# Kernel tuning notes

Measured on AMD Instinct MI355X. Metric: run time of the kernel, lower is better.

## Reference

```python
import jax, jax.numpy as jnp
import numpy as np

B, T, D = 4, 2048, 1024

def setup_inputs() -> dict:
    key = jax.random.key(0)
    kx, kq, kk, kv = jax.random.split(key, 4)
    return {
        "vector": jax.random.normal(kx, (B, T, D), dtype=jnp.float32),
        # original uses torch.rand -> uniform [0,1)
        "W_queries": jax.random.uniform(kq, (D, D), dtype=jnp.float32),
        "W_keys": jax.random.uniform(kk, (D, D), dtype=jnp.float32),
        "W_values": jax.random.uniform(kv, (D, D), dtype=jnp.float32),
    }

def reference(vector, W_queries, W_keys, W_values):
    b, num_token, d_out = vector.shape
    queries = vector @ W_queries          # [b, t, d]
    keys = vector @ W_keys                # [b, t, d]
    values = vector @ W_values            # [b, t, d]
    # attention_score: [b, q, k]
    scores = jnp.einsum('bqd,bkd->bqk', queries, keys)
    causal_mask = jnp.triu(jnp.ones((num_token, num_token), dtype=bool), k=1)
    scores = jnp.where(causal_mask[None, :, :], -jnp.inf, scores)
    # NOTE: original uses FLOOR division `//` by sqrt(d_k) -- faithful here.
    inv_sqrt_scale = jnp.asarray(np.sqrt(keys.shape[-1]), dtype=scores.dtype)
    weights = jnp.floor(scores / inv_sqrt_scale)
    # NOTE: original applies softmax over dim=1 (the query axis), not dim=-1.
    weights = jax.nn.softmax(weights, axis=1)
    # dropout rate is 0.0 (eval/deterministic): identity
    context = jnp.einsum('bqk,bkd->bqd', weights, values)
    return context
```

## Files before the change

kernel.cpp:

```cpp
#include <hip/hip_runtime.h>
#include <math.h>

typedef _Float16 half4 __attribute__((ext_vector_type(4)));
typedef _Float16 half8 __attribute__((ext_vector_type(8)));
typedef float f32x4 __attribute__((ext_vector_type(4)));

#define GLD16(gptr, lptr)                                                     \
    __builtin_amdgcn_global_load_lds(                                         \
        (const __attribute__((address_space(1))) unsigned int*)(gptr),        \
        (__attribute__((address_space(3))) unsigned int*)(lptr), 16, 0, 0)

namespace {

constexpr int Bb = 4;
constexpr int Tt = 2048;
constexpr int Dd = 1024;
constexpr int BT = Bb * Tt;
constexpr int NCH = 16;

__device__ inline _Float16 f2h(float f) { return (_Float16)f; }

__global__ __launch_bounds__(256) void convert_x_kernel(
    const float* __restrict__ X, _Float16* __restrict__ Xhi, _Float16* __restrict__ Xlo)
{
    const int idx = (blockIdx.x * 256 + threadIdx.x) * 4;
    const float4 v = *(const float4*)(X + idx);
    const float a[4] = {v.x, v.y, v.z, v.w};
    half4 h, l;
#pragma unroll
    for (int i = 0; i < 4; ++i) {
        h[i] = f2h(a[i]);
        l[i] = f2h(a[i] - (float)h[i]);
    }
    *(half4*)(Xhi + idx) = h;
    *(half4*)(Xlo + idx) = l;
}

__global__ __launch_bounds__(256) void convert_wqk_kernel(
    const float* __restrict__ Wq, const float* __restrict__ Wk,
    _Float16* __restrict__ Wqh, _Float16* __restrict__ Wql,
    _Float16* __restrict__ Wkh, _Float16* __restrict__ Wkl)
{
    const int mat = blockIdx.y;
    const float* W = mat ? Wk : Wq;
    _Float16* Hh = mat ? Wkh : Wqh;
    _Float16* Ll = mat ? Wkl : Wql;
    const int idx = (blockIdx.x * 256 + threadIdx.x) * 4;
    const float4 v = *(const float4*)(W + idx);
    const float a[4] = {v.x, v.y, v.z, v.w};
    half4 h, l;
#pragma unroll
    for (int i = 0; i < 4; ++i) {
        h[i] = f2h(a[i]);
        l[i] = f2h(a[i] - (float)h[i]);
    }
    *(half4*)(Hh + idx) = h;
    *(half4*)(Ll + idx) = l;
}

__global__ __launch_bounds__(256) void convert_wv_kernel(
    const float* __restrict__ Wv, _Float16* __restrict__ WvTh)
{
    __shared__ float tile[64][65];
    const int n0 = blockIdx.x * 64, k0 = blockIdx.y * 64;
    const int tx = threadIdx.x & 63, ty = threadIdx.x >> 6;
#pragma unroll
    for (int i = 0; i < 16; ++i)
        tile[ty + i * 4][tx] = Wv[(size_t)(k0 + ty + i * 4) * Dd + n0 + tx];
    __syncthreads();
#pragma unroll
    for (int i = 0; i < 16; ++i) {
        const float v = tile[tx][ty + i * 4];
        WvTh[(size_t)(n0 + ty + i * 4) * Dd + k0 + tx] = f2h(v);
    }
}

__global__ __launch_bounds__(256) void gt_kernel(
    const _Float16* __restrict__ Wkh, const _Float16* __restrict__ Wkl,
    const _Float16* __restrict__ Wqh, const _Float16* __restrict__ Wql,
    _Float16* __restrict__ GTh, _Float16* __restrict__ GTl)
{
    __shared__ _Float16 Ahl[2][4][512];
    __shared__ _Float16 Bhl[2][4][512];

    const int n0 = blockIdx.x * 64;
    const int m0 = blockIdx.y * 64;
    const int tid = threadIdx.x;
    const int w = tid >> 6, lane = tid & 63;
    const int lr = lane & 15, lq = lane >> 4;
    const int wi = (w >> 1) * 2, wj = (w & 1) * 2;

    f32x4 acc[2][2];
#pragma unroll
    for (int i = 0; i < 2; ++i)
#pragma unroll
        for (int j = 0; j < 2; ++j)
#pragma unroll
            for (int c = 0; c < 4; ++c) acc[i][j][c] = 0.f;

    for (int kk = 0; kk < 1024; kk += 32) {
        __syncthreads();
        {
            const int s = w;
            const size_t ar = (size_t)(m0 + s * 16 + lr) * Dd + kk + lq * 8;
            const size_t br = (size_t)(n0 + s * 16 + lr) * Dd + kk + lq * 8;
            GLD16(Wkh + ar, &Ahl[0][s][0]);
            GLD16(Wkl + ar, &Ahl[1][s][0]);
            GLD16(Wqh + br, &Bhl[0][s][0]);
            GLD16(Wql + br, &Bhl[1][s][0]);
        }
        __syncthreads();
        half8 ah[2], al[2], bh[2], bl[2];
#pragma unroll
        for (int i = 0; i < 2; ++i) {
            ah[i] = *(const half8*)&Ahl[0][wi + i][lane * 8];
            al[i] = *(const half8*)&Ahl[1][wi + i][lane * 8];
        }
#pragma unroll
        for (int j = 0; j < 2; ++j) {
            bh[j] = *(const half8*)&Bhl[0][wj + j][lane * 8];
            bl[j] = *(const half8*)&Bhl[1][wj + j][lane * 8];
        }
#pragma unroll
        for (int i = 0; i < 2; ++i)
#pragma unroll
            for (int j = 0; j < 2; ++j) {
                acc[i][j] = __builtin_amdgcn_mfma_f32_16x16x32_f16(ah[i], bh[j], acc[i][j], 0, 0, 0);
                acc[i][j] = __builtin_amdgcn_mfma_f32_16x16x32_f16(ah[i], bl[j], acc[i][j], 0, 0, 0);
                acc[i][j] = __builtin_amdgcn_mfma_f32_16x16x32_f16(al[i], bh[j], acc[i][j], 0, 0, 0);
            }
    }

#pragma unroll
    for (int i = 0; i < 2; ++i)
#pragma unroll
        for (int r = 0; r < 4; ++r) {
            const int row = m0 + (wi + i) * 16 + lq * 4 + r;
#pragma unroll
            for (int j = 0; j < 2; ++j) {
                const int col = n0 + (wj + j) * 16 + lr;
                const float v = acc[i][j][r];
                const _Float16 h = f2h(v);
                GTh[(size_t)row * Dd + col] = h;
                GTl[(size_t)row * Dd + col] = f2h(v - (float)h);
            }
        }
}

__global__ __launch_bounds__(256) void t_kernel(
    const _Float16* __restrict__ Xhi, const _Float16* __restrict__ Xlo,
    const _Float16* __restrict__ GTh, const _Float16* __restrict__ GTl,
    _Float16* __restrict__ Thi, _Float16* __restrict__ Tlo)
{
    __shared__ _Float16 Ahl[2][8][512];
    __shared__ _Float16 Bhl[2][8][512];

    const int n0 = blockIdx.x * 128;
    const int m0 = blockIdx.y * 128;
    const int tid = threadIdx.x;
    const int w = tid >> 6, lane = tid & 63;
    const int lr = lane & 15, lq = lane >> 4;
    const int wr = (w >> 1) * 4, wc = (w & 1) * 4;

    f32x4 acc[4][4];
#pragma unroll
    for (int i = 0; i < 4; ++i)
#pragma unroll
        for (int j = 0; j < 4; ++j)
#pragma unroll
            for (int c = 0; c < 4; ++c) acc[i][j][c] = 0.f;

    for (int kk = 0; kk < 1024; kk += 32) {
        __syncthreads();
#pragma unroll
        for (int s2 = 0; s2 < 2; ++s2) {
            const int s = w * 2 + s2;
            const size_t ar = (size_t)(m0 + s * 16 + lr) * Dd + kk + lq * 8;
            const size_t br = (size_t)(n0 + s * 16 + lr) * Dd + kk + lq * 8;
            GLD16(Xhi + ar, &Ahl[0][s][0]);
            GLD16(Xlo + ar, &Ahl[1][s][0]);
            GLD16(GTh + br, &Bhl[0][s][0]);
            GLD16(GTl + br, &Bhl[1][s][0]);
        }
        __syncthreads();
        half8 ah[4], al[4], bh[4], bl[4];
#pragma unroll
        for (int i = 0; i < 4; ++i) {
            ah[i] = *(const half8*)&Ahl[0][wr + i][lane * 8];
            al[i] = *(const half8*)&Ahl[1][wr + i][lane * 8];
        }
#pragma unroll
        for (int j = 0; j < 4; ++j) {
            bh[j] = *(const half8*)&Bhl[0][wc + j][lane * 8];
            bl[j] = *(const half8*)&Bhl[1][wc + j][lane * 8];
        }
#pragma unroll
        for (int i = 0; i < 4; ++i)
#pragma unroll
            for (int j = 0; j < 4; ++j) {
                acc[i][j] = __builtin_amdgcn_mfma_f32_16x16x32_f16(ah[i], bh[j], acc[i][j], 0, 0, 0);
                acc[i][j] = __builtin_amdgcn_mfma_f32_16x16x32_f16(ah[i], bl[j], acc[i][j], 0, 0, 0);
                acc[i][j] = __builtin_amdgcn_mfma_f32_16x16x32_f16(al[i], bh[j], acc[i][j], 0, 0, 0);
            }
    }
#pragma unroll
    for (int i = 0; i < 4; ++i)
#pragma unroll
        for (int r = 0; r < 4; ++r) {
            const int row = m0 + (wr + i) * 16 + lq * 4 + r;
#pragma unroll
            for (int j = 0; j < 4; ++j) {
                const int col = n0 + (wc + j) * 16 + lr;
                const float v = acc[i][j][r];
                const _Float16 h = f2h(v);
                Thi[(size_t)row * Dd + col] = h;
                Tlo[(size_t)row * Dd + col] = f2h(v - (float)h);
            }
        }
}

__global__ __launch_bounds__(256) void v_kernel(
    const _Float16* __restrict__ Xhi, const _Float16* __restrict__ WvTh,
    _Float16* __restrict__ Vrow)
{
    __shared__ _Float16 Al[8][512];
    __shared__ _Float16 Bl[8][512];

    const int n0 = blockIdx.x * 128;
    const int m0 = blockIdx.y * 128;
    const int tid = threadIdx.x;
    const int w = tid >> 6, lane = tid & 63;
    const int lr = lane & 15, lq = lane >> 4;
    const int wr = (w >> 1) * 4, wc = (w & 1) * 4;

    f32x4 acc[4][4];
#pragma unroll
    for (int i = 0; i < 4; ++i)
#pragma unroll
        for (int j = 0; j < 4; ++j)
#pragma unroll
            for (int c = 0; c < 4; ++c) acc[i][j][c] = 0.f;

    for (int kk = 0; kk < 1024; kk += 32) {
        __syncthreads();
#pragma unroll
        for (int s2 = 0; s2 < 2; ++s2) {
            const int s = w * 2 + s2;
            GLD16(Xhi + (size_t)(m0 + s * 16 + lr) * Dd + kk + lq * 8, &Al[s][0]);
            GLD16(WvTh + (size_t)(n0 + s * 16 + lr) * Dd + kk + lq * 8, &Bl[s][0]);
        }
        __syncthreads();
        half8 a[4], b2[4];
#pragma unroll
        for (int i = 0; i < 4; ++i) a[i] = *(const half8*)&Al[wr + i][lane * 8];
#pragma unroll
        for (int j = 0; j < 4; ++j) b2[j] = *(const half8*)&Bl[wc + j][lane * 8];
#pragma unroll
        for (int i = 0; i < 4; ++i)
#pragma unroll
            for (int j = 0; j < 4; ++j)
                acc[i][j] = __builtin_amdgcn_mfma_f32_16x16x32_f16(a[i], b2[j], acc[i][j], 0, 0, 0);
    }
#pragma unroll
    for (int i = 0; i < 4; ++i)
#pragma unroll
        for (int r = 0; r < 4; ++r) {
            const int row = m0 + (wr + i) * 16 + lq * 4 + r;
#pragma unroll
            for (int j = 0; j < 4; ++j)
                Vrow[(size_t)row * Dd + n0 + (wc + j) * 16 + lr] = f2h(acc[i][j][r]);
        }
}

__global__ __launch_bounds__(256) void transpose_v_kernel(
    const _Float16* __restrict__ Vrow, const float* __restrict__ Lb,
    _Float16* __restrict__ Vt)
{
    __shared__ _Float16 tile[64][78];
    const int d0 = blockIdx.x * 64, t0 = blockIdx.y * 64, b = blockIdx.z;
    const int tx = threadIdx.x & 63, ty = threadIdx.x >> 6;
#pragma unroll
    for (int i = 0; i < 16; ++i)
        tile[ty + i * 4][tx] = Vrow[((size_t)b * Tt + t0 + ty + i * 4) * Dd + d0 + tx];
    __syncthreads();
    const float sc = Lb[(size_t)b * Tt + t0 + tx];
#pragma unroll
    for (int i = 0; i < 16; ++i) {
        const float v = (float)tile[tx][ty + i * 4] * sc;
        Vt[(size_t)b * Dd * Tt + (size_t)(d0 + ty + i * 4) * Tt + t0 + tx] = f2h(v);
    }
}

__global__ __launch_bounds__(256) void scores_mfma_kernel(
    const _Float16* __restrict__ Thi, const _Float16* __restrict__ Tlo,
    const _Float16* __restrict__ Xhi, const _Float16* __restrict__ Xlo,
    float* __restrict__ S, float* __restrict__ Pm, float* __restrict__ Pl)
{
    const int t = blockIdx.x;
    int byi = (int)((sqrtf(8.f * t + 1.f) - 1.f) * 0.5f);
    if ((byi + 1) * (byi + 2) / 2 <= t) ++byi;
    if (byi * (byi + 1) / 2 > t) --byi;
    const int bxi = t - byi * (byi + 1) / 2;
    const int b = blockIdx.z;
    const int j0 = bxi * 128, q0 = byi * 128;
    float* Sb = S + (size_t)b * Tt * Tt;

    __shared__ _Float16 Ahl[2][8][512];
    __shared__ _Float16 Bhl[2][8][512];
    const _Float16* Th = Thi + (size_t)b * Tt * Dd;
    const _Float16* Tl = Tlo + (size_t)b * Tt * Dd;
    const _Float16* Xh = Xhi + (size_t)b * Tt * Dd;
    const _Float16* Xl = Xlo + (size_t)b * Tt * Dd;

    const int tid = threadIdx.x;
    const int w = tid >> 6, lane = tid & 63;
    const int lr = lane & 15, lq = lane >> 4;
    const int wr = (w >> 1) * 4, wc = (w & 1) * 4;

    f32x4 acc[4][4];
#pragma unroll
    for (int i = 0; i < 4; ++i)
#pragma unroll
        for (int j = 0; j < 4; ++j)
#pragma unroll
            for (int c = 0; c < 4; ++c) acc[i][j][c] = 0.f;

    for (int kk = 0; kk < 1024; kk += 32) {
        __syncthreads();
#pragma unroll
        for (int s2 = 0; s2 < 2; ++s2) {
            const int s = w * 2 + s2;
            const size_t ar = (size_t)(q0 + s * 16 + lr) * Dd + kk + lq * 8;
            const size_t br = (size_t)(j0 + s * 16 + lr) * Dd + kk + lq * 8;
            GLD16(Th + ar, &Ahl[0][s][0]);
            GLD16(Tl + ar, &Ahl[1][s][0]);
            GLD16(Xh + br, &Bhl[0][s][0]);
            GLD16(Xl + br, &Bhl[1][s][0]);
        }
        __syncthreads();
        half8 ah[4], al[4], bh[4], bl[4];
#pragma unroll
        for (int i = 0; i < 4; ++i) {
            ah[i] = *(const half8*)&Ahl[0][wr + i][lane * 8];
            al[i] = *(const half8*)&Ahl[1][wr + i][lane * 8];
        }
#pragma unroll
        for (int j = 0; j < 4; ++j) {
            bh[j] = *(const half8*)&Bhl[0][wc + j][lane * 8];
            bl[j] = *(const half8*)&Bhl[1][wc + j][lane * 8];
        }
#pragma unroll
        for (int i = 0; i < 4; ++i)
#pragma unroll
            for (int j = 0; j < 4; ++j) {
                acc[i][j] = __builtin_amdgcn_mfma_f32_16x16x32_f16(ah[i], bh[j], acc[i][j], 0, 0, 0);
                acc[i][j] = __builtin_amdgcn_mfma_f32_16x16x32_f16(ah[i], bl[j], acc[i][j], 0, 0, 0);
                acc[i][j] = __builtin_amdgcn_mfma_f32_16x16x32_f16(al[i], bh[j], acc[i][j], 0, 0, 0);
            }
    }

    float sv[4][4][4];
#pragma unroll
    for (int i = 0; i < 4; ++i)
#pragma unroll
        for (int r = 0; r < 4; ++r) {
            const int q = q0 + (wr + i) * 16 + lq * 4 + r;
#pragma unroll
            for (int j = 0; j < 4; ++j) {
                const int jg = j0 + (wc + j) * 16 + lr;
                const float v = (jg <= q) ? floorf(acc[i][j][r] * 0.03125f) : -INFINITY;
                sv[i][j][r] = v;
                Sb[(size_t)q * Tt + jg] = v;
            }
        }

    float* red  = (float*)&Ahl[0][0][0];
    float* colm = red + 2048;
    __syncthreads();
    for (int e = tid; e < 2048; e += 256) red[e] = -INFINITY;
    __syncthreads();
    const int rowidx = (w * 4 + lq) * 128;
#pragma unroll
    for (int j = 0; j < 4; ++j) {
        const int c = (wc + j) * 16 + lr;
        float lm = -INFINITY;
#pragma unroll
        for (int i = 0; i < 4; ++i)
#pragma unroll
            for (int r = 0; r < 4; ++r) lm = fmaxf(lm, sv[i][j][r]);
        red[rowidx + c] = lm;
    }
    __syncthreads();
    if (tid < 128) {
        float m = -INFINITY;
#pragma unroll
        for (int e = 0; e < 16; ++e) m = fmaxf(m, red[e * 128 + tid]);
        colm[tid] = m;
    }
    __syncthreads();
    float ls[4];
#pragma unroll
    for (int j = 0; j < 4; ++j) {
        const int c = (wc + j) * 16 + lr;
        const float m = colm[c];
        float s = 0.f;
#pragma unroll
        for (int i = 0; i < 4; ++i)
#pragma unroll
            for (int r = 0; r < 4; ++r)
                if (sv[i][j][r] != -INFINITY) s += __expf(sv[i][j][r] - m);
        ls[j] = s;
    }
    __syncthreads();
    for (int e = tid; e < 2048; e += 256) red[e] = 0.f;
    __syncthreads();
#pragma unroll
    for (int j = 0; j < 4; ++j) red[rowidx + (wc + j) * 16 + lr] = ls[j];
    __syncthreads();
    if (tid < 128) {
        float l = 0.f;
#pragma unroll
        for (int e = 0; e < 16; ++e) l += red[e * 128 + tid];
        const size_t o = ((size_t)b * NCH + byi) * Tt + j0 + tid;
        Pm[o] = colm[tid];
        Pl[o] = l;
    }
}

__global__ __launch_bounds__(256) void colstats_merge_kernel(
    const float* __restrict__ Pm, const float* __restrict__ Pl,
    float* __restrict__ Mb, float* __restrict__ Lb)
{
    const int j = blockIdx.x * 256 + threadIdx.x;
    const int b = blockIdx.y;
    const int jt = j >> 7;
    float m = -INFINITY, l = 0.f;
    for (int c = jt; c < NCH; ++c) {
        const size_t pidx = ((size_t)b * NCH + c) * Tt + j;
        const float mi = Pm[pidx];
        if (mi == -INFINITY) continue;
        const float li = Pl[pidx];
        if (mi > m) { l = l * __expf(m - mi) + li; m = mi; }
        else        { l += li * __expf(mi - m); }
    }
    Mb[(size_t)b * Tt + j] = m;
    Lb[(size_t)b * Tt + j] = (l > 0.f) ? 1.f / l : 0.f;
}

__global__ __launch_bounds__(256) void pmat_kernel(
    const float* __restrict__ S, const float* __restrict__ Mb,
    _Float16* __restrict__ P)
{
    const int t = blockIdx.x;
    int byi = (int)((sqrtf(8.f * t + 1.f) - 1.f) * 0.5f);
    if ((byi + 1) * (byi + 2) / 2 <= t) ++byi;
    if (byi * (byi + 1) / 2 > t) --byi;
    const int bxi = t - byi * (byi + 1) / 2;
    const int b = blockIdx.z;
    const int j0 = bxi * 128, q0 = byi * 128;

    const int tr = threadIdx.x >> 4;
    const int tc = (threadIdx.x & 15) * 8;
    const float* mp = Mb + (size_t)b * Tt + j0 + tc;
    float mv[8];
#pragma unroll
    for (int e = 0; e < 8; ++e) mv[e] = mp[e];

#pragma unroll
    for (int it = 0; it < 8; ++it) {
        const int row = q0 + it * 16 + tr;
        const float* Sp = S + (size_t)b * Tt * Tt + (size_t)row * Tt + j0 + tc;
        const float4 s0 = *(const float4*)Sp;
        const float4 s1 = *(const float4*)(Sp + 4);
        const float sa[8] = {s0.x, s0.y, s0.z, s0.w, s1.x, s1.y, s1.z, s1.w};
        half8 out;
#pragma unroll
        for (int e = 0; e < 8; ++e) {
            const int jg = j0 + tc + e;
            out[e] = (jg <= row) ? f2h(__expf(sa[e] - mv[e])) : (_Float16)0.f;
        }
        *(half8*)(P + (size_t)b * Tt * Tt + (size_t)row * Tt + j0 + tc) = out;
    }
}

__global__ __launch_bounds__(256) void context_mfma_kernel(
    const _Float16* __restrict__ P, const _Float16* __restrict__ Vt,
    float* __restrict__ Out)
{
    __shared__ _Float16 Al[8][512];
    __shared__ _Float16 Bl[8][512];

    const int bx = blockIdx.x;
    const int by = (int)gridDim.y - 1 - blockIdx.y;
    const int b  = blockIdx.z;
    const int d0 = bx * 128;
    const int q0 = by * 128;
    const _Float16* Pb = P + (size_t)b * Tt * Tt;
    const _Float16* Vb = Vt + (size_t)b * Dd * Tt;
    float* Ob = Out + (size_t)b * Tt * Dd;

    const int tid = threadIdx.x;
    const int w = tid >> 6, lane = tid & 63;
    const int lr = lane & 15, lq = lane >> 4;
    const int wr = (w >> 1) * 4, wc = (w & 1) * 4;

    f32x4 acc[4][4];
#pragma unroll
    for (int i = 0; i < 4; ++i)
#pragma unroll
        for (int j = 0; j < 4; ++j)
#pragma unroll
            for (int c = 0; c < 4; ++c) acc[i][j][c] = 0.f;

    const int kmax = q0 + 128;
    for (int k0 = 0; k0 < kmax; k0 += 32) {
        __syncthreads();
#pragma unroll
        for (int s2 = 0; s2 < 2; ++s2) {
            const int s = w * 2 + s2;
            GLD16(Pb + (size_t)(q0 + s * 16 + lr) * Tt + k0 + lq * 8, &Al[s][0]);
            GLD16(Vb + (size_t)(d0 + s * 16 + lr) * Tt + k0 + lq * 8, &Bl[s][0]);
        }
        __syncthreads();
        half8 a[4], b2[4];
#pragma unroll
        for (int i = 0; i < 4; ++i) a[i] = *(const half8*)&Al[wr + i][lane * 8];
#pragma unroll
        for (int j = 0; j < 4; ++j) b2[j] = *(const half8*)&Bl[wc + j][lane * 8];
#pragma unroll
        for (int i = 0; i < 4; ++i)
#pragma unroll
            for (int j = 0; j < 4; ++j)
                acc[i][j] = __builtin_amdgcn_mfma_f32_16x16x32_f16(a[i], b2[j], acc[i][j], 0, 0, 0);
    }

#pragma unroll
    for (int i = 0; i < 4; ++i)
#pragma unroll
        for (int r = 0; r < 4; ++r) {
            const int row = q0 + (wr + i) * 16 + lq * 4 + r;
#pragma unroll
            for (int j = 0; j < 4; ++j)
                Ob[(size_t)row * Dd + d0 + (wc + j) * 16 + lr] = acc[i][j][r];
        }
}

}

extern "C" void kernel_launch(void* const* d_in, const int* in_sizes, int n_in,
                              void* d_out, int out_size, void* d_ws, size_t ws_size,
                              hipStream_t stream)
{
    const float* X  = (const float*)d_in[0];
    const float* Wq = (const float*)d_in[1];
    const float* Wk = (const float*)d_in[2];
    const float* Wv = (const float*)d_in[3];

    char* ws = (char*)d_ws;
    const size_t MB = 1024 * 1024;
    _Float16* Xhi  = (_Float16*)ws;
    _Float16* Xlo  = (_Float16*)(ws + 16 * MB);
    _Float16* Wqh  = (_Float16*)(ws + 32 * MB);
    _Float16* Wql  = (_Float16*)(ws + 34 * MB);
    _Float16* Wkh  = (_Float16*)(ws + 36 * MB);
    _Float16* Wkl  = (_Float16*)(ws + 38 * MB);
    _Float16* WvTh = (_Float16*)(ws + 40 * MB);
    _Float16* GTh  = (_Float16*)(ws + 44 * MB);
    _Float16* GTl  = (_Float16*)(ws + 46 * MB);
    _Float16* Thi  = (_Float16*)(ws + 48 * MB);
    _Float16* Tlo  = (_Float16*)(ws + 64 * MB);
    _Float16* P    = Thi;
    _Float16* Vt   = (_Float16*)(ws + 80 * MB);
    _Float16* Vrow = (_Float16*)(ws + 96 * MB);
    float*    S    = (float*)(ws + 112 * MB);
    float*    Mb   = (float*)(ws + 176 * MB);
    float*    Lb   = Mb + (size_t)Bb * Tt;
    float*    Pm   = Lb + (size_t)Bb * Tt;
    float*    Pl   = Pm + (size_t)Bb * NCH * Tt;
    float*    Out  = (float*)d_out;

    convert_x_kernel<<<BT * Dd / 1024, 256, 0, stream>>>(X, Xhi, Xlo);
    convert_wqk_kernel<<<dim3(Dd * Dd / 1024, 2), 256, 0, stream>>>(Wq, Wk, Wqh, Wql, Wkh, Wkl);
    convert_wv_kernel<<<dim3(16, 16), 256, 0, stream>>>(Wv, WvTh);
    gt_kernel<<<dim3(16, 16), 256, 0, stream>>>(Wkh, Wkl, Wqh, Wql, GTh, GTl);
    t_kernel<<<dim3(8, 64), 256, 0, stream>>>(Xhi, Xlo, GTh, GTl, Thi, Tlo);
    v_kernel<<<dim3(8, 64), 256, 0, stream>>>(Xhi, WvTh, Vrow);
    scores_mfma_kernel<<<dim3(136, 1, Bb), 256, 0, stream>>>(Thi, Tlo, Xhi, Xlo, S, Pm, Pl);
    colstats_merge_kernel<<<dim3(Tt / 256, Bb), 256, 0, stream>>>(Pm, Pl, Mb, Lb);
    transpose_v_kernel<<<dim3(Dd / 64, Tt / 64, Bb), 256, 0, stream>>>(Vrow, Lb, Vt);
    pmat_kernel<<<dim3(136, 1, Bb), 256, 0, stream>>>(S, Mb, P);
    context_mfma_kernel<<<dim3(Dd / 128, Tt / 128, Bb), 256, 0, stream>>>(P, Vt, Out);
}
```

Baseline: 456.2 us.

## Double-buffer LDS tiles in all MFMA GEMM kernels to overlap loads with compute

Each MFMA GEMM kernel (gt, t, v, scores, context) now keeps two LDS buffers. It issues the global-to-LDS load for the next K slice before computing on the current one, and the two barriers per iteration become one waitcnt+barrier. This hides global load latency behind MFMA work and removes a barrier per step. In exchange LDS use doubles (up to 64KB for the hi/lo kernels), which can lower occupancy.

```diff
diff --git a/kernel.cpp b/kernel.cpp
--- a/kernel.cpp
+++ b/kernel.cpp
@@ -9,6 +9,12 @@
     __builtin_amdgcn_global_load_lds(                                         \
         (const __attribute__((address_space(1))) unsigned int*)(gptr),        \
         (__attribute__((address_space(3))) unsigned int*)(lptr), 16, 0, 0)
+
+#define PIPE_SYNC()                                                           \
+    do {                                                                      \
+        asm volatile("s_waitcnt vmcnt(0)" ::: "memory");                      \
+        __builtin_amdgcn_s_barrier();                                         \
+    } while (0)
 
 namespace {
 
@@ -80,8 +86,8 @@
     const _Float16* __restrict__ Wqh, const _Float16* __restrict__ Wql,
     _Float16* __restrict__ GTh, _Float16* __restrict__ GTl)
 {
-    __shared__ _Float16 Ahl[2][4][512];
-    __shared__ _Float16 Bhl[2][4][512];
+    __shared__ _Float16 Ahl[2][2][4][512];
+    __shared__ _Float16 Bhl[2][2][4][512];
 
     const int n0 = blockIdx.x * 64;
     const int m0 = blockIdx.y * 64;
@@ -98,28 +104,31 @@
 #pragma unroll
             for (int c = 0; c < 4; ++c) acc[i][j][c] = 0.f;
 
-    for (int kk = 0; kk < 1024; kk += 32) {
-        __syncthreads();
-        {
-            const int s = w;
-            const size_t ar = (size_t)(m0 + s * 16 + lr) * Dd + kk + lq * 8;
-            const size_t br = (size_t)(n0 + s * 16 + lr) * Dd + kk + lq * 8;
-            GLD16(Wkh + ar, &Ahl[0][s][0]);
-            GLD16(Wkl + ar, &Ahl[1][s][0]);
-            GLD16(Wqh + br, &Bhl[0][s][0]);
-            GLD16(Wql + br, &Bhl[1][s][0]);
-        }
-        __syncthreads();
+    auto stage = [&](int bf, int kk) {
+        const int s = w;
+        const size_t ar = (size_t)(m0 + s * 16 + lr) * Dd + kk + lq * 8;
+        const size_t br = (size_t)(n0 + s * 16 + lr) * Dd + kk + lq * 8;
+        GLD16(Wkh + ar, &Ahl[bf][0][s][0]);
+        GLD16(Wkl + ar, &Ahl[bf][1][s][0]);
+        GLD16(Wqh + br, &Bhl[bf][0][s][0]);
+        GLD16(Wql + br, &Bhl[bf][1][s][0]);
+    };
+
+    stage(0, 0);
+    PIPE_SYNC();
+    int ib = 0;
+    for (int kk = 0; kk < 1024; kk += 32, ib ^= 1) {
+        if (kk + 32 < 1024) stage(ib ^ 1, kk + 32);
         half8 ah[2], al[2], bh[2], bl[2];
 #pragma unroll
         for (int i = 0; i < 2; ++i) {
-            ah[i] = *(const half8*)&Ahl[0][wi + i][lane * 8];
-            al[i] = *(const half8*)&Ahl[1][wi + i][lane * 8];
+            ah[i] = *(const half8*)&Ahl[ib][0][wi + i][lane * 8];
+            al[i] = *(const half8*)&Ahl[ib][1][wi + i][lane * 8];
         }
 #pragma unroll
         for (int j = 0; j < 2; ++j) {
-            bh[j] = *(const half8*)&Bhl[0][wj + j][lane * 8];
-            bl[j] = *(const half8*)&Bhl[1][wj + j][lane * 8];
+            bh[j] = *(const half8*)&Bhl[ib][0][wj + j][lane * 8];
+            bl[j] = *(const half8*)&Bhl[ib][1][wj + j][lane * 8];
         }
 #pragma unroll
         for (int i = 0; i < 2; ++i)
@@ -129,6 +138,7 @@
                 acc[i][j] = __builtin_amdgcn_mfma_f32_16x16x32_f16(ah[i], bl[j], acc[i][j], 0, 0, 0);
                 acc[i][j] = __builtin_amdgcn_mfma_f32_16x16x32_f16(al[i], bh[j], acc[i][j], 0, 0, 0);
             }
+        PIPE_SYNC();
     }
 
 #pragma unroll
@@ -152,8 +162,8 @@
     const _Float16* __restrict__ GTh, const _Float16* __restrict__ GTl,
     _Float16* __restrict__ Thi, _Float16* __restrict__ Tlo)
 {
-    __shared__ _Float16 Ahl[2][8][512];
-    __shared__ _Float16 Bhl[2][8][512];
+    __shared__ _Float16 Ahl[2][2][8][512];
+    __shared__ _Float16 Bhl[2][2][8][512];
 
     const int n0 = blockIdx.x * 128;
     const int m0 = blockIdx.y * 128;
@@ -170,29 +180,34 @@
 #pragma unroll
             for (int c = 0; c < 4; ++c) acc[i][j][c] = 0.f;
 
-    for (int kk = 0; kk < 1024; kk += 32) {
-        __syncthreads();
+    auto stage = [&](int bf, int kk) {
 #pragma unroll
         for (int s2 = 0; s2 < 2; ++s2) {
             const int s = w * 2 + s2;
             const size_t ar = (size_t)(m0 + s * 16 + lr) * Dd + kk + lq * 8;
             const size_t br = (size_t)(n0 + s * 16 + lr) * Dd + kk + lq * 8;
-            GLD16(Xhi + ar, &Ahl[0][s][0]);
-            GLD16(Xlo + ar, &Ahl[1][s][0]);
-            GLD16(GTh + br, &Bhl[0][s][0]);
-            GLD16(GTl + br, &Bhl[1][s][0]);
-        }
-        __syncthreads();
+            GLD16(Xhi + ar, &Ahl[bf][0][s][0]);
+            GLD16(Xlo + ar, &Ahl[bf][1][s][0]);
+            GLD16(GTh + br, &Bhl[bf][0][s][0]);
+            GLD16(GTl + br, &Bhl[bf][1][s][0]);
+        }
+    };
+
+    stage(0, 0);
+    PIPE_SYNC();
+    int ib = 0;
+    for (int kk = 0; kk < 1024; kk += 32, ib ^= 1) {
+        if (kk + 32 < 1024) stage(ib ^ 1, kk + 32);
         half8 ah[4], al[4], bh[4], bl[4];
 #pragma unroll
         for (int i = 0; i < 4; ++i) {
-            ah[i] = *(const half8*)&Ahl[0][wr + i][lane * 8];
-            al[i] = *(const half8*)&Ahl[1][wr + i][lane * 8];
+            ah[i] = *(const half8*)&Ahl[ib][0][wr + i][lane * 8];
+            al[i] = *(const half8*)&Ahl[ib][1][wr + i][lane * 8];
         }
 #pragma unroll
         for (int j = 0; j < 4; ++j) {
-            bh[j] = *(const half8*)&Bhl[0][wc + j][lane * 8];
-            bl[j] = *(const half8*)&Bhl[1][wc + j][lane * 8];
+            bh[j] = *(const half8*)&Bhl[ib][0][wc + j][lane * 8];
+            bl[j] = *(const half8*)&Bhl[ib][1][wc + j][lane * 8];
         }
 #pragma unroll
         for (int i = 0; i < 4; ++i)
@@ -202,6 +217,7 @@
                 acc[i][j] = __builtin_amdgcn_mfma_f32_16x16x32_f16(ah[i], bl[j], acc[i][j], 0, 0, 0);
                 acc[i][j] = __builtin_amdgcn_mfma_f32_16x16x32_f16(al[i], bh[j], acc[i][j], 0, 0, 0);
             }
+        PIPE_SYNC();
     }
 #pragma unroll
     for (int i = 0; i < 4; ++i)
@@ -223,8 +239,8 @@
     const _Float16* __restrict__ Xhi, const _Float16* __restrict__ WvTh,
     _Float16* __restrict__ Vrow)
 {
-    __shared__ _Float16 Al[8][512];
-    __shared__ _Float16 Bl[8][512];
+    __shared__ _Float16 Al[2][8][512];
+    __shared__ _Float16 Bl[2][8][512];
 
     const int n0 = blockIdx.x * 128;
     const int m0 = blockIdx.y * 128;
@@ -241,25 +257,31 @@
 #pragma unroll
             for (int c = 0; c < 4; ++c) acc[i][j][c] = 0.f;
 
-    for (int kk = 0; kk < 1024; kk += 32) {
-        __syncthreads();
+    auto stage = [&](int bf, int kk) {
 #pragma unroll
         for (int s2 = 0; s2 < 2; ++s2) {
             const int s = w * 2 + s2;
-            GLD16(Xhi + (size_t)(m0 + s * 16 + lr) * Dd + kk + lq * 8, &Al[s][0]);
-            GLD16(WvTh + (size_t)(n0 + s * 16 + lr) * Dd + kk + lq * 8, &Bl[s][0]);
-        }
-        __syncthreads();
+            GLD16(Xhi + (size_t)(m0 + s * 16 + lr) * Dd + kk + lq * 8, &Al[bf][s][0]);
+            GLD16(WvTh + (size_t)(n0 + s * 16 + lr) * Dd + kk + lq * 8, &Bl[bf][s][0]);
+        }
+    };
+
+    stage(0, 0);
+    PIPE_SYNC();
+    int ib = 0;
+    for (int kk = 0; kk < 1024; kk += 32, ib ^= 1) {
+        if (kk + 32 < 1024) stage(ib ^ 1, kk + 32);
         half8 a[4], b2[4];
 #pragma unroll
-        for (int i = 0; i < 4; ++i) a[i] = *(const half8*)&Al[wr + i][lane * 8];
-#pragma unroll
-        for (int j = 0; j < 4; ++j) b2[j] = *(const half8*)&Bl[wc + j][lane * 8];
+        for (int i = 0; i < 4; ++i) a[i] = *(const half8*)&Al[ib][wr + i][lane * 8];
+#pragma unroll
+        for (int j = 0; j < 4; ++j) b2[j] = *(const half8*)&Bl[ib][wc + j][lane * 8];
 #pragma unroll
         for (int i = 0; i < 4; ++i)
 #pragma unroll
             for (int j = 0; j < 4; ++j)
                 acc[i][j] = __builtin_amdgcn_mfma_f32_16x16x32_f16(a[i], b2[j], acc[i][j], 0, 0, 0);
+        PIPE_SYNC();
     }
 #pragma unroll
     for (int i = 0; i < 4; ++i)
@@ -305,8 +327,8 @@
     const int j0 = bxi * 128, q0 = byi * 128;
     float* Sb = S + (size_t)b * Tt * Tt;
 
-    __shared__ _Float16 Ahl[2][8][512];
-    __shared__ _Float16 Bhl[2][8][512];
+    __shared__ _Float16 Ahl[2][2][8][512];
+    __shared__ _Float16 Bhl[2][2][8][512];
     const _Float16* Th = Thi + (size_t)b * Tt * Dd;
     const _Float16* Tl = Tlo + (size_t)b * Tt * Dd;
     const _Float16* Xh = Xhi + (size_t)b * Tt * Dd;
@@ -325,29 +347,34 @@
 #pragma unroll
             for (int c = 0; c < 4; ++c) acc[i][j][c] = 0.f;
 
-    for (int kk = 0; kk < 1024; kk += 32) {
-        __syncthreads();
+    auto stage = [&](int bf, int kk) {
 #pragma unroll
         for (int s2 = 0; s2 < 2; ++s2) {
             const int s = w * 2 + s2;
             const size_t ar = (size_t)(q0 + s * 16 + lr) * Dd + kk + lq * 8;
             const size_t br = (size_t)(j0 + s * 16 + lr) * Dd + kk + lq * 8;
-            GLD16(Th + ar, &Ahl[0][s][0]);
-            GLD16(Tl + ar, &Ahl[1][s][0]);
-            GLD16(Xh + br, &Bhl[0][s][0]);
-            GLD16(Xl + br, &Bhl[1][s][0]);
-        }
-        __syncthreads();
+            GLD16(Th + ar, &Ahl[bf][0][s][0]);
+            GLD16(Tl + ar, &Ahl[bf][1][s][0]);
+            GLD16(Xh + br, &Bhl[bf][0][s][0]);
+            GLD16(Xl + br, &Bhl[bf][1][s][0]);
+        }
+    };
+
+    stage(0, 0);
+    PIPE_SYNC();
+    int ib = 0;
+    for (int kk = 0; kk < 1024; kk += 32, ib ^= 1) {
+        if (kk + 32 < 1024) stage(ib ^ 1, kk + 32);
         half8 ah[4], al[4], bh[4], bl[4];
 #pragma unroll
         for (int i = 0; i < 4; ++i) {
-            ah[i] = *(const half8*)&Ahl[0][wr + i][lane * 8];
-            al[i] = *(const half8*)&Ahl[1][wr + i][lane * 8];
+            ah[i] = *(const half8*)&Ahl[ib][0][wr + i][lane * 8];
+            al[i] = *(const half8*)&Ahl[ib][1][wr + i][lane * 8];
         }
 #pragma unroll
         for (int j = 0; j < 4; ++j) {
-            bh[j] = *(const half8*)&Bhl[0][wc + j][lane * 8];
-            bl[j] = *(const half8*)&Bhl[1][wc + j][lane * 8];
+            bh[j] = *(const half8*)&Bhl[ib][0][wc + j][lane * 8];
+            bl[j] = *(const half8*)&Bhl[ib][1][wc + j][lane * 8];
         }
 #pragma unroll
         for (int i = 0; i < 4; ++i)
@@ -357,6 +384,7 @@
                 acc[i][j] = __builtin_amdgcn_mfma_f32_16x16x32_f16(ah[i], bl[j], acc[i][j], 0, 0, 0);
                 acc[i][j] = __builtin_amdgcn_mfma_f32_16x16x32_f16(al[i], bh[j], acc[i][j], 0, 0, 0);
             }
+        PIPE_SYNC();
     }
 
     float sv[4][4][4];
@@ -374,7 +402,7 @@
             }
         }
 
-    float* red  = (float*)&Ahl[0][0][0];
+    float* red  = (float*)&Ahl[0][0][0][0];
     float* colm = red + 2048;
     __syncthreads();
     for (int e = tid; e < 2048; e += 256) red[e] = -INFINITY;
@@ -487,8 +515,8 @@
     const _Float16* __restrict__ P, const _Float16* __restrict__ Vt,
     float* __restrict__ Out)
 {
-    __shared__ _Float16 Al[8][512];
-    __shared__ _Float16 Bl[8][512];
+    __shared__ _Float16 Al[2][8][512];
+    __shared__ _Float16 Bl[2][8][512];
 
     const int bx = blockIdx.x;
     const int by = (int)gridDim.y - 1 - blockIdx.y;
@@ -512,26 +540,32 @@
 #pragma unroll
             for (int c = 0; c < 4; ++c) acc[i][j][c] = 0.f;
 
-    const int kmax = q0 + 128;
-    for (int k0 = 0; k0 < kmax; k0 += 32) {
-        __syncthreads();
+    auto stage = [&](int bf, int k0) {
 #pragma unroll
         for (int s2 = 0; s2 < 2; ++s2) {
             const int s = w * 2 + s2;
-            GLD16(Pb + (size_t)(q0 + s * 16 + lr) * Tt + k0 + lq * 8, &Al[s][0]);
-            GLD16(Vb + (size_t)(d0 + s * 16 + lr) * Tt + k0 + lq * 8, &Bl[s][0]);
-        }
-        __syncthreads();
+            GLD16(Pb + (size_t)(q0 + s * 16 + lr) * Tt + k0 + lq * 8, &Al[bf][s][0]);
+            GLD16(Vb + (size_t)(d0 + s * 16 + lr) * Tt + k0 + lq * 8, &Bl[bf][s][0]);
+        }
+    };
+
+    const int kmax = q0 + 128;
+    stage(0, 0);
+    PIPE_SYNC();
+    int ib = 0;
+    for (int k0 = 0; k0 < kmax; k0 += 32, ib ^= 1) {
+        if (k0 + 32 < kmax) stage(ib ^ 1, k0 + 32);
         half8 a[4], b2[4];
 #pragma unroll
-        for (int i = 0; i < 4; ++i) a[i] = *(const half8*)&Al[wr + i][lane * 8];
-#pragma unroll
-        for (int j = 0; j < 4; ++j) b2[j] = *(const half8*)&Bl[wc + j][lane * 8];
+        for (int i = 0; i < 4; ++i) a[i] = *(const half8*)&Al[ib][wr + i][lane * 8];
+#pragma unroll
+        for (int j = 0; j < 4; ++j) b2[j] = *(const half8*)&Bl[ib][wc + j][lane * 8];
 #pragma unroll
         for (int i = 0; i < 4; ++i)
 #pragma unroll
             for (int j = 0; j < 4; ++j)
                 acc[i][j] = __builtin_amdgcn_mfma_f32_16x16x32_f16(a[i], b2[j], acc[i][j], 0, 0, 0);
+        PIPE_SYNC();
     }
 
 #pragma unroll
```

Result: no change. 451.6 us (-1.0%).
